# Kernel tuning notes

Measured on AMD Instinct MI355X. Metric: run time of the kernel, lower is better.

Reference implementation:

```python
import jax, jax.numpy as jnp
import numpy as np

EPS = 1e-8
PAD = 1  # kernel // 2 for kernel=3


def setup_inputs() -> dict:
    key = jax.random.key(0)
    k1, k2, k3, k4, k5 = jax.random.split(key, 5)
    b, c, h, w = 16, 256, 64, 64
    out_ch, kernel, style_dim = 256, 3, 512
    x = jax.random.normal(k1, (b, c, h, w), dtype=jnp.float32)
    style = jax.random.normal(k2, (b, style_dim), dtype=jnp.float32)
    # learned params
    weight = jax.random.normal(k3, (1, out_ch, c, kernel, kernel), dtype=jnp.float32)
    lim = 1.0 / np.sqrt(style_dim)
    mod_w = jax.random.uniform(k4, (c, style_dim), minval=-lim, maxval=lim, dtype=jnp.float32)
    mod_b = jax.random.uniform(k5, (c,), minval=-lim, maxval=lim, dtype=jnp.float32)
    return {"x": x, "style": style, "weight": weight, "mod_w": mod_w, "mod_b": mod_b}


def reference(x, style, weight, mod_w, mod_b):
    # s[b,i]: per-sample, per-input-channel modulation from the style Linear
    s = style @ mod_w.T + mod_b                     # [b, in_ch]
    w = weight[0]                                    # [out_ch, in_ch, k, k]
    # demod factor: sum_{i,kh,kw} (w[o,i,kh,kw]*s[b,i])^2 = sum_i s^2 * sum_kk w^2
    w_sq = jnp.sum(w * w, axis=(2, 3))               # [out_ch, in_ch]
    d = jax.lax.rsqrt(jnp.einsum('oi,bi->bo', w_sq, s * s) + EPS)  # [b, out_ch]
    # modulate input channels instead of materializing per-sample weights
    xs = x * s[:, :, None, None]                     # [b, in_ch, h, w]
    y = jax.lax.conv_general_dilated(
        xs, w, window_strides=(1, 1), padding=[(PAD, PAD), (PAD, PAD)],
        dimension_numbers=('NCHW', 'OIHW', 'NCHW'))
    return y * d[:, :, None, None]                   # [b, out_ch, h, w]
```

## Files before the change

kernel.cpp:

```cpp
#include <hip/hip_runtime.h>
#include <hip/hip_bf16.h>
#include <cstdint>
#include <cstddef>

typedef __bf16 bf16_t;
typedef __bf16 bf16x4 __attribute__((ext_vector_type(4)));
typedef __bf16 bf16x8 __attribute__((ext_vector_type(8)));
typedef float  f32x4  __attribute__((ext_vector_type(4)));

#define NB   16
#define NC   256
#define NO   256
#define SD   512
#define NPIX 4096
#define CPAD 40

#define WS_S   0
#define WS_D   16384
#define WS_WSQ 32768
#define WS_WT  294912

__global__ __launch_bounds__(256) void prep1(
    const float* __restrict__ style, const float* __restrict__ weight,
    const float* __restrict__ mod_w, const float* __restrict__ mod_b,
    float* __restrict__ s_buf, float* __restrict__ wsq, bf16_t* __restrict__ wT)
{
    const int blk = blockIdx.x;
    const int tid = threadIdx.x;
    if (blk < 16) {
        const int b = blk, i = tid;
        const float* st = style + b * SD;
        const float* mw = mod_w + i * SD;
        float acc = 0.f;
        for (int k = 0; k < SD; k += 4) {
            float4 a = *(const float4*)(st + k);
            float4 c = *(const float4*)(mw + k);
            acc += a.x * c.x + a.y * c.y + a.z * c.z + a.w * c.w;
        }
        s_buf[b * NC + i] = acc + mod_b[i];
    } else {
        const int o = blk - 16, i = tid;
        const float* wp = weight + (o * NC + i) * 9;
        float q = 0.f;
        #pragma unroll
        for (int t = 0; t < 9; ++t) {
            float v = wp[t];
            q += v * v;
            wT[t * (NO * NC) + o * NC + i] = (bf16_t)v;
        }
        wsq[o * NC + i] = q;
    }
}

__global__ __launch_bounds__(256) void prep2(
    const float* __restrict__ s_buf, const float* __restrict__ wsq,
    float* __restrict__ d_buf)
{
    const int b = blockIdx.x, o = threadIdx.x;
    const float* wq = wsq + o * NC;
    const float* sb = s_buf + b * NC;
    float sum = 0.f;
    for (int i = 0; i < NC; ++i) {
        float sv = sb[i];
        sum += wq[i] * sv * sv;
    }
    d_buf[b * NC + o] = rsqrtf(sum + 1e-8f);
}

__device__ __forceinline__ void stage_a(const bf16_t* __restrict__ wT_tap,
                                        int o0, int ic0, bf16_t* dst, int tid)
{
    #pragma unroll
    for (int it = 0; it < 2; ++it) {
        int s = it * 256 + tid;
        const bf16_t* g = wT_tap + (o0 + (s & 127)) * NC + ic0 + (s >> 7) * 8;
        __builtin_amdgcn_global_load_lds(
            (const __attribute__((address_space(1))) void*)g,
            (__attribute__((address_space(3))) void*)(dst + s * 8),
            16, 0, 0);
    }
}

__global__ __launch_bounds__(256, 3) void conv_mfma(
    const float* __restrict__ x,
    const bf16_t* __restrict__ wT,
    const float* __restrict__ s_buf,
    const float* __restrict__ d_buf,
    float* __restrict__ out)
{
    __shared__ bf16_t lds_a[2][4096];
    __shared__ bf16_t lds_b[4 * 64 * CPAD];

    const int tid   = threadIdx.x;
    const int lane  = tid & 63;
    const int wv    = tid >> 6;
    const int wo    = wv >> 1;
    const int wp    = wv & 1;
    const int pt    = blockIdx.x;
    const int o0    = blockIdx.y * 128;
    const int batch = blockIdx.z;
    const int row0  = pt * 2;

    const int l15 = lane & 15;
    const int kg  = lane >> 4;
    const int k0  = kg * 8;

    const int colB = tid & 63;
    const int cgrp = tid >> 6;

    f32x4 acc[4][4];
    #pragma unroll
    for (int i = 0; i < 4; ++i)
        #pragma unroll
        for (int j = 0; j < 4; ++j) {
            f32x4 z = {0.f, 0.f, 0.f, 0.f};
            acc[i][j] = z;
        }

    bf16x8 bzero;
    #pragma unroll
    for (int j = 0; j < 8; ++j) bzero[j] = (bf16_t)0.f;

    auto STAGE = [&](int ic0) {
        const float* sp = s_buf + batch * NC + ic0 + cgrp * 8;
        float4 sa = *(const float4*)sp;
        float4 sb = *(const float4*)(sp + 4);
        float sv[8] = {sa.x, sa.y, sa.z, sa.w, sb.x, sb.y, sb.z, sb.w};
        const float* xbase = x + (size_t)(batch * NC + ic0 + cgrp * 8) * NPIX + colB;
        #pragma unroll
        for (int rh = 0; rh < 2; ++rh) {
            float v[2][8];
            #pragma unroll
            for (int rr = 0; rr < 2; ++rr) {
                const int r = rh * 2 + rr;
                const int gy = row0 - 1 + r;
                const bool valid = ((unsigned)gy < 64u);
                const float* rp = xbase + gy * 64;
                #pragma unroll
                for (int j = 0; j < 8; ++j)
                    v[rr][j] = valid ? rp[j * NPIX] : 0.f;
            }
            #pragma unroll
            for (int rr = 0; rr < 2; ++rr) {
                const int r = rh * 2 + rr;
                union { bf16_t h[8]; uint4 u; } pk;
                #pragma unroll
                for (int j = 0; j < 8; ++j)
                    pk.h[j] = (bf16_t)(v[rr][j] * sv[j]);
                *(uint4*)&lds_b[(r * 64 + colB) * CPAD + cgrp * 8] = pk.u;
            }
        }
    };

    const size_t TSTR = (size_t)NO * NC;

    for (int chunk = 0; chunk < 8; ++chunk) {
        const int ic0 = chunk * 32;

        STAGE(ic0);
        stage_a(wT, o0, ic0, &lds_a[0][0], tid);
        __syncthreads();

        #pragma unroll
        for (int tap = 0; tap < 9; ++tap) {
            if (tap < 8)
                stage_a(wT + (size_t)(tap + 1) * TSTR, o0, ic0,
                        &lds_a[(tap + 1) & 1][0], tid);

            const bf16_t* abuf = &lds_a[tap & 1][0];
            const int kh = tap / 3, kw = tap % 3;

            bf16x8 af[4];
            #pragma unroll
            for (int of = 0; of < 4; ++of)
                af[of] = *(const bf16x8*)&abuf[kg * 1024 + (wo * 64 + of * 16 + l15) * 8];

            const int r = wp + kh;
            bf16x8 bfr[4];
            #pragma unroll
            for (int nf = 0; nf < 4; ++nf) {
                const int c = nf * 16 + l15 + kw - 1;
                if ((unsigned)c < 64u) {
                    bfr[nf] = *(const bf16x8*)&lds_b[(r * 64 + c) * CPAD + k0];
                } else {
                    bfr[nf] = bzero;
                }
            }

            #pragma unroll
            for (int of = 0; of < 4; ++of)
                #pragma unroll
                for (int nf = 0; nf < 4; ++nf)
                    acc[of][nf] = __builtin_amdgcn_mfma_f32_16x16x32_bf16(
                        af[of], bfr[nf], acc[of][nf], 0, 0, 0);

            __syncthreads();
        }
    }

    const int p_base = pt * 128 + wp * 64;
    #pragma unroll
    for (int of = 0; of < 4; ++of) {
        #pragma unroll
        for (int rg = 0; rg < 4; ++rg) {
            const int o_g = o0 + wo * 64 + of * 16 + (lane >> 4) * 4 + rg;
            const float dv = d_buf[batch * NO + o_g];
            const size_t obase = (size_t)(batch * NO + o_g) * NPIX;
            #pragma unroll
            for (int nf = 0; nf < 4; ++nf) {
                const int p_g = p_base + nf * 16 + l15;
                out[obase + p_g] = acc[of][nf][rg] * dv;
            }
        }
    }
}

extern "C" void kernel_launch(void* const* d_in, const int* in_sizes, int n_in,
                              void* d_out, int out_size, void* d_ws, size_t ws_size,
                              hipStream_t stream)
{
    const float* x      = (const float*)d_in[0];
    const float* style  = (const float*)d_in[1];
    const float* weight = (const float*)d_in[2];
    const float* mod_w  = (const float*)d_in[3];
    const float* mod_b  = (const float*)d_in[4];
    float* out = (float*)d_out;

    char* ws = (char*)d_ws;
    float*  s_buf = (float*)(ws + WS_S);
    float*  d_buf = (float*)(ws + WS_D);
    float*  wsq   = (float*)(ws + WS_WSQ);
    bf16_t* wT    = (bf16_t*)(ws + WS_WT);

    hipLaunchKernelGGL(prep1, dim3(272), dim3(256), 0, stream,
                       style, weight, mod_w, mod_b, s_buf, wsq, wT);
    hipLaunchKernelGGL(prep2, dim3(16), dim3(256), 0, stream, s_buf, wsq, d_buf);
    hipLaunchKernelGGL(conv_mfma, dim3(32, 2, 16), dim3(256), 0, stream,
                       x, wT, s_buf, d_buf, out);
}
```

Measured before the change: 278.2 us.

## Deepen weight prefetch pipeline, prefetch next x chunk, fuse demod into conv

Weight tiles now go through a 4-deep LDS ring with a 2-tap lookahead that crosses chunk boundaries. Ordering uses explicit vmcnt/lgkmcnt waits and raw barriers instead of __syncthreads after every tap. The next input-channel chunk of x is loaded into registers while the current chunk's MFMAs run, then written to LDS with padding 36 instead of 40. The demodulation factor is now computed at the end of the conv kernel, which removes the prep2 launch. In exchange, register and LDS pressure rise and occupancy drops to 2 blocks per SM.

```diff
diff --git a/kernel.cpp b/kernel.cpp
--- a/kernel.cpp
+++ b/kernel.cpp
@@ -13,10 +13,9 @@
 #define NO   256
 #define SD   512
 #define NPIX 4096
-#define CPAD 40
+#define CPAD 36
 
 #define WS_S   0
-#define WS_D   16384
 #define WS_WSQ 32768
 #define WS_WT  294912
 
@@ -52,21 +51,6 @@
     }
 }
 
-__global__ __launch_bounds__(256) void prep2(
-    const float* __restrict__ s_buf, const float* __restrict__ wsq,
-    float* __restrict__ d_buf)
-{
-    const int b = blockIdx.x, o = threadIdx.x;
-    const float* wq = wsq + o * NC;
-    const float* sb = s_buf + b * NC;
-    float sum = 0.f;
-    for (int i = 0; i < NC; ++i) {
-        float sv = sb[i];
-        sum += wq[i] * sv * sv;
-    }
-    d_buf[b * NC + o] = rsqrtf(sum + 1e-8f);
-}
-
 __device__ __forceinline__ void stage_a(const bf16_t* __restrict__ wT_tap,
                                         int o0, int ic0, bf16_t* dst, int tid)
 {
@@ -81,14 +65,14 @@
     }
 }
 
-__global__ __launch_bounds__(256, 3) void conv_mfma(
+__global__ __launch_bounds__(256, 2) void conv_mfma(
     const float* __restrict__ x,
     const bf16_t* __restrict__ wT,
     const float* __restrict__ s_buf,
-    const float* __restrict__ d_buf,
+    const float* __restrict__ wsq,
     float* __restrict__ out)
 {
-    __shared__ bf16_t lds_a[2][4096];
+    __shared__ bf16_t lds_a[4][4096];
     __shared__ bf16_t lds_b[4 * 64 * CPAD];
 
     const int tid   = threadIdx.x;
@@ -121,53 +105,73 @@
     #pragma unroll
     for (int j = 0; j < 8; ++j) bzero[j] = (bf16_t)0.f;
 
-    auto STAGE = [&](int ic0) {
+    const size_t TSTR = (size_t)NO * NC;
+    bf16_t* lds_a0 = &lds_a[0][0];
+
+    float vx[4][8];
+    float sv[8];
+    auto XLOAD = [&](int ic0) {
         const float* sp = s_buf + batch * NC + ic0 + cgrp * 8;
         float4 sa = *(const float4*)sp;
         float4 sb = *(const float4*)(sp + 4);
-        float sv[8] = {sa.x, sa.y, sa.z, sa.w, sb.x, sb.y, sb.z, sb.w};
+        sv[0]=sa.x; sv[1]=sa.y; sv[2]=sa.z; sv[3]=sa.w;
+        sv[4]=sb.x; sv[5]=sb.y; sv[6]=sb.z; sv[7]=sb.w;
         const float* xbase = x + (size_t)(batch * NC + ic0 + cgrp * 8) * NPIX + colB;
         #pragma unroll
-        for (int rh = 0; rh < 2; ++rh) {
-            float v[2][8];
-            #pragma unroll
-            for (int rr = 0; rr < 2; ++rr) {
-                const int r = rh * 2 + rr;
-                const int gy = row0 - 1 + r;
-                const bool valid = ((unsigned)gy < 64u);
-                const float* rp = xbase + gy * 64;
+        for (int r = 0; r < 4; ++r) {
+            const int gy = row0 - 1 + r;
+            const bool valid = ((unsigned)gy < 64u);
+            const float* rp = xbase + gy * 64;
+            #pragma unroll
+            for (int j = 0; j < 8; ++j)
+                vx[r][j] = valid ? rp[j * NPIX] : 0.f;
+        }
+    };
+    auto BWRITE = [&]() {
+        #pragma unroll
+        for (int r = 0; r < 4; ++r) {
+            const int lbase = (r * 64 + colB) * CPAD + cgrp * 8;
+            #pragma unroll
+            for (int half = 0; half < 2; ++half) {
+                union { bf16_t h[4]; uint2 u; } pk;
                 #pragma unroll
-                for (int j = 0; j < 8; ++j)
-                    v[rr][j] = valid ? rp[j * NPIX] : 0.f;
-            }
-            #pragma unroll
-            for (int rr = 0; rr < 2; ++rr) {
-                const int r = rh * 2 + rr;
-                union { bf16_t h[8]; uint4 u; } pk;
-                #pragma unroll
-                for (int j = 0; j < 8; ++j)
-                    pk.h[j] = (bf16_t)(v[rr][j] * sv[j]);
-                *(uint4*)&lds_b[(r * 64 + colB) * CPAD + cgrp * 8] = pk.u;
+                for (int j = 0; j < 4; ++j)
+                    pk.h[j] = (bf16_t)(vx[r][half * 4 + j] * sv[half * 4 + j]);
+                *(uint2*)&lds_b[lbase + half * 4] = pk.u;
             }
         }
     };
 
-    const size_t TSTR = (size_t)NO * NC;
-
+    XLOAD(0);
+    BWRITE();
+    stage_a(wT,        o0, 0, lds_a0 + 0 * 4096, tid);
+    stage_a(wT + TSTR, o0, 0, lds_a0 + 1 * 4096, tid);
+    asm volatile("s_waitcnt lgkmcnt(0)" ::: "memory");
+    __builtin_amdgcn_sched_barrier(0);
+    __builtin_amdgcn_s_barrier();
+
+    #pragma unroll 1
     for (int chunk = 0; chunk < 8; ++chunk) {
         const int ic0 = chunk * 32;
 
-        STAGE(ic0);
-        stage_a(wT, o0, ic0, &lds_a[0][0], tid);
-        __syncthreads();
-
         #pragma unroll
         for (int tap = 0; tap < 9; ++tap) {
-            if (tap < 8)
-                stage_a(wT + (size_t)(tap + 1) * TSTR, o0, ic0,
-                        &lds_a[(tap + 1) & 1][0], tid);
-
-            const bf16_t* abuf = &lds_a[tap & 1][0];
+            bf16_t* nbuf = lds_a0 + (size_t)((chunk + tap + 2) & 3) * 4096;
+            if (tap < 7) {
+                stage_a(wT + (size_t)(tap + 2) * TSTR, o0, ic0, nbuf, tid);
+                asm volatile("s_waitcnt vmcnt(4)" ::: "memory");
+            } else if (chunk < 7) {
+                stage_a(wT + (size_t)(tap - 7) * TSTR, o0, ic0 + 32, nbuf, tid);
+                asm volatile("s_waitcnt vmcnt(4)" ::: "memory");
+            } else if (tap == 7) {
+                asm volatile("s_waitcnt vmcnt(2)" ::: "memory");
+            } else {
+                asm volatile("s_waitcnt vmcnt(0)" ::: "memory");
+            }
+            __builtin_amdgcn_sched_barrier(0);
+            __builtin_amdgcn_s_barrier();
+
+            const bf16_t* abuf = lds_a0 + (size_t)((chunk + tap) & 3) * 4096;
             const int kh = tap / 3, kw = tap % 3;
 
             bf16x8 af[4];
@@ -181,7 +185,10 @@
             for (int nf = 0; nf < 4; ++nf) {
                 const int c = nf * 16 + l15 + kw - 1;
                 if ((unsigned)c < 64u) {
-                    bfr[nf] = *(const bf16x8*)&lds_b[(r * 64 + c) * CPAD + k0];
+                    const bf16_t* p = &lds_b[(r * 64 + c) * CPAD + k0];
+                    bf16x4 lo = *(const bf16x4*)p;
+                    bf16x4 hi = *(const bf16x4*)(p + 4);
+                    bfr[nf] = __builtin_shufflevector(lo, hi, 0, 1, 2, 3, 4, 5, 6, 7);
                 } else {
                     bfr[nf] = bzero;
                 }
@@ -193,19 +200,47 @@
                 for (int nf = 0; nf < 4; ++nf)
                     acc[of][nf] = __builtin_amdgcn_mfma_f32_16x16x32_bf16(
                         af[of], bfr[nf], acc[of][nf], 0, 0, 0);
-
-            __syncthreads();
-        }
-    }
+        }
+
+        if (chunk < 7) {
+            XLOAD(ic0 + 32);
+            __builtin_amdgcn_sched_barrier(0);
+            __builtin_amdgcn_s_barrier();
+            BWRITE();
+            asm volatile("s_waitcnt lgkmcnt(0)" ::: "memory");
+            __builtin_amdgcn_sched_barrier(0);
+            __builtin_amdgcn_s_barrier();
+        }
+    }
+
+    __syncthreads();
+    float* d_sh = (float*)&lds_b[0];
+    {
+        const int ol   = tid >> 1;
+        const int half = tid & 1;
+        const float* wq = wsq + (size_t)(o0 + ol) * NC + half * 128;
+        const float* sb = s_buf + batch * NC + half * 128;
+        float sum = 0.f;
+        #pragma unroll 4
+        for (int i = 0; i < 128; i += 4) {
+            float4 w4 = *(const float4*)(wq + i);
+            float4 s4 = *(const float4*)(sb + i);
+            sum += w4.x * s4.x * s4.x + w4.y * s4.y * s4.y
+                 + w4.z * s4.z * s4.z + w4.w * s4.w * s4.w;
+        }
+        sum += __shfl_xor(sum, 1);
+        if (half == 0) d_sh[ol] = rsqrtf(sum + 1e-8f);
+    }
+    __syncthreads();
 
     const int p_base = pt * 128 + wp * 64;
     #pragma unroll
     for (int of = 0; of < 4; ++of) {
         #pragma unroll
         for (int rg = 0; rg < 4; ++rg) {
-            const int o_g = o0 + wo * 64 + of * 16 + (lane >> 4) * 4 + rg;
-            const float dv = d_buf[batch * NO + o_g];
-            const size_t obase = (size_t)(batch * NO + o_g) * NPIX;
+            const int o_l = wo * 64 + of * 16 + (lane >> 4) * 4 + rg;
+            const float dv = d_sh[o_l];
+            const size_t obase = (size_t)(batch * NO + o0 + o_l) * NPIX;
             #pragma unroll
             for (int nf = 0; nf < 4; ++nf) {
                 const int p_g = p_base + nf * 16 + l15;
@@ -228,13 +263,11 @@
 
     char* ws = (char*)d_ws;
     float*  s_buf = (float*)(ws + WS_S);
-    float*  d_buf = (float*)(ws + WS_D);
     float*  wsq   = (float*)(ws + WS_WSQ);
     bf16_t* wT    = (bf16_t*)(ws + WS_WT);
 
     hipLaunchKernelGGL(prep1, dim3(272), dim3(256), 0, stream,
                        style, weight, mod_w, mod_b, s_buf, wsq, wT);
-    hipLaunchKernelGGL(prep2, dim3(16), dim3(256), 0, stream, s_buf, wsq, d_buf);
     hipLaunchKernelGGL(conv_mfma, dim3(32, 2, 16), dim3(256), 0, stream,
-                       x, wT, s_buf, d_buf, out);
-}
+                       x, wT, s_buf, wsq, out);
+}
```

Result: faster. 235.1 us (-15.5%).
